# Optimization experiments

Hardware: AMD Instinct MI355X
Metric: run time of the kernel (lower is better)

## Reference

```python
import jax, jax.numpy as jnp
import numpy as np

N, D_IM, D_CLI = 2048, 1024, 64
EPS = 1e-12  # F.normalize eps


def setup_inputs() -> dict:
    key = jax.random.key(0)
    k1, k2, k3, k4 = jax.random.split(key, 4)
    phi_im = jax.random.normal(k1, (N, D_IM), dtype=jnp.float32)
    phi_cli = jax.random.normal(k2, (N, D_CLI), dtype=jnp.float32)
    t = jax.random.randint(k3, (N, 2), 0, 3, dtype=jnp.int64)
    traumatic = jax.random.randint(k4, (N,), 0, 2, dtype=jnp.int64)
    return {"phi_im": phi_im, "phi_cli": phi_cli, "t": t, "traumatic": traumatic}


def _l2norm(x):
    n = jnp.sqrt(jnp.sum(x * x, axis=1, keepdims=True))
    return x / jnp.maximum(n, EPS)


def _pair_block(S, ma, mb):
    # S: [N,N] full cosine similarity; ma, mb: [N] bool group masks.
    valid = ma[:, None] & mb[None, :]
    mat = jnp.where(valid, S, 0.0)            # scatter-into-zero matrix semantics
    masked = jnp.where(valid, S, jnp.inf)     # masked argmin = nearest (least similar) pair
    flat = jnp.argmin(masked.reshape(-1))
    i = flat // S.shape[1]
    j = flat % S.shape[1]
    return mat, masked.reshape(-1)[flat], jnp.stack([i, j])


def reference(phi_im, phi_cli, t, traumatic):
    im_n = _l2norm(phi_im)
    cli_n = _l2norm(phi_cli)
    # single batched GEMM replaces the per-pair python loops
    S_im = im_n @ im_n.T    # [N,N]
    S_cli = cli_n @ cli_n.T  # [N,N]

    t1 = t[:, 1]
    m0 = (t1 == 0) & (traumatic == 1)
    m1 = t1 == 1
    m2 = t1 == 2

    mats, vals, idxs = [], [], []
    for S in (S_im, S_cli):
        for (ma, mb) in ((m0, m1), (m0, m2), (m1, m2)):
            mat, v, ij = _pair_block(S, ma, mb)
            mats.append(mat)
            vals.append(v)
            idxs.append(ij)
    sims = jnp.stack(mats)           # [6, N, N]: im_01, im_02, im_12, cli_01, cli_02, cli_12
    min_vals = jnp.stack(vals)       # [6]
    min_idx = jnp.stack(idxs)        # [6, 2]
    return sims, min_vals, min_idx
```

## Files before the change

### kernel.cpp

```cpp
#include <hip/hip_runtime.h>
#include <stdint.h>

#define NROW 2048
#define D_IM 1024
#define D_CLI 64
#define EPSF 1e-12f
#define NN ((size_t)NROW * (size_t)NROW)

typedef __attribute__((ext_vector_type(8))) short bf16x8;
typedef __attribute__((ext_vector_type(4))) float f32x4;

#define OFF_PACKED   0
#define OFF_CNT      64
#define OFF_CAT      128
#define OFF_LISTS    8320
#define OFF_POS      32896
#define OFF_COLINFO  41216
#define OFF_INVIM    65792
#define OFF_INVCLI   73984
#define OFF_PIM      82176
#define OFF_PCLI     8470784
#define OFF_SC       8995072

__device__ __forceinline__ unsigned int enc_f32(float x) {
    unsigned int u = __float_as_uint(x);
    return (u & 0x80000000u) ? ~u : (u | 0x80000000u);
}
__device__ __forceinline__ unsigned short bf16rn(float x) {
    unsigned int u = __float_as_uint(x);
    return (unsigned short)((u + 0x7FFFu + ((u >> 16) & 1u)) >> 16);
}
__device__ __forceinline__ float bf16tof(unsigned short h) {
    return __uint_as_float(((unsigned int)h) << 16);
}

__global__ __launch_bounds__(256)
void prepscan_kernel(const float* __restrict__ phi_im,
                     const float* __restrict__ phi_cli,
                     const int* __restrict__ t,
                     const int* __restrict__ traumatic,
                     float* __restrict__ inv_im,
                     float* __restrict__ inv_cli,
                     char* __restrict__ pim,
                     char* __restrict__ pcli,
                     int* __restrict__ cnt,
                     int* __restrict__ catArr,
                     int* __restrict__ lists,
                     int* __restrict__ posIn,
                     unsigned int* __restrict__ colinfo,
                     unsigned long long* __restrict__ packed) {
    __shared__ unsigned long long shmem[256];
    const int tid = threadIdx.x;

    if (blockIdx.x == NROW) {
        int cats[8];
        unsigned long long mycnt = 0;
        #pragma unroll
        for (int e = 0; e < 8; e++) {
            int r = tid * 8 + e;
            int t1 = t[2 * r + 1];
            int tr = traumatic[r];
            int c = (t1 == 1) ? 1 : ((t1 == 2) ? 2 : ((tr == 1) ? 0 : 3));
            cats[e] = c;
            catArr[r] = c;
            if (c < 3) mycnt += 1ULL << (21 * c);
        }
        shmem[tid] = mycnt;
        __syncthreads();
        for (int off = 1; off < 256; off <<= 1) {
            unsigned long long v = (tid >= off) ? shmem[tid - off] : 0ULL;
            __syncthreads();
            shmem[tid] += v;
            __syncthreads();
        }
        unsigned long long excl = shmem[tid] - mycnt;
        unsigned long long tot = shmem[255];
        unsigned int loc[3];
        #pragma unroll
        for (int c = 0; c < 3; c++)
            loc[c] = (unsigned int)(excl >> (21 * c)) & 0x1FFFFFu;
        #pragma unroll
        for (int e = 0; e < 8; e++) {
            int r = tid * 8 + e;
            int c = cats[e];
            unsigned int slot = 0xFFFFFFFFu;
            if (c < 3) {
                slot = loc[c]++;
                lists[c * 2048 + slot] = r;
                posIn[r] = (int)slot;
            }
            colinfo[0 * 2048 + r] = (c == 1) ? slot : 0xFFFFFFFFu;
            colinfo[1 * 2048 + r] = (c == 2) ? slot : 0xFFFFFFFFu;
            colinfo[2 * 2048 + r] = (c == 2) ? slot : 0xFFFFFFFFu;
        }
        if (tid == 0) {
            cnt[0] = (int)(tot & 0x1FFFFFu);
            cnt[1] = (int)((tot >> 21) & 0x1FFFFFu);
            cnt[2] = (int)((tot >> 42) & 0x1FFFFFu);
            cnt[3] = 0;
        }
        if (tid < 6) packed[tid] = 0xFFFFFFFFFFFFFFFFULL;
        return;
    }

    float* sred = (float*)shmem;
    const int r = blockIdx.x;

    float4 v = ((const float4*)(phi_im + (size_t)r * D_IM))[tid];
    float a[4] = {v.x, v.y, v.z, v.w};
    unsigned short h4[4], l4[4];
    #pragma unroll
    for (int e = 0; e < 4; e++) {
        h4[e] = bf16rn(a[e]);
        l4[e] = bf16rn(a[e] - bf16tof(h4[e]));
    }
    {
        char* rowb = pim + (size_t)r * 4096 + (tid >> 1) * 32 + (tid & 1) * 8;
        *(ushort4*)rowb = make_ushort4(h4[0], h4[1], h4[2], h4[3]);
        *(ushort4*)(rowb + 16) = make_ushort4(l4[0], l4[1], l4[2], l4[3]);
    }
    sred[tid] = a[0] * a[0] + a[1] * a[1] + a[2] * a[2] + a[3] * a[3];
    __syncthreads();
    for (int off = 128; off > 0; off >>= 1) {
        if (tid < off) sred[tid] += sred[tid + off];
        __syncthreads();
    }
    if (tid == 0) inv_im[r] = 1.0f / fmaxf(sqrtf(sred[0]), EPSF);

    if (tid < 16) {
        float4 c = ((const float4*)(phi_cli + (size_t)r * D_CLI))[tid];
        float b[4] = {c.x, c.y, c.z, c.w};
        unsigned short ch[4], cl[4];
        #pragma unroll
        for (int e = 0; e < 4; e++) {
            ch[e] = bf16rn(b[e]);
            cl[e] = bf16rn(b[e] - bf16tof(ch[e]));
        }
        char* rowb = pcli + (size_t)r * 256 + (tid >> 1) * 32 + (tid & 1) * 8;
        *(ushort4*)rowb = make_ushort4(ch[0], ch[1], ch[2], ch[3]);
        *(ushort4*)(rowb + 16) = make_ushort4(cl[0], cl[1], cl[2], cl[3]);
    }
    if (tid < 64) {
        float c = phi_cli[(size_t)r * D_CLI + tid];
        float cs = c * c;
        #pragma unroll
        for (int off = 32; off > 0; off >>= 1) cs += __shfl_down(cs, off, 64);
        if (tid == 0) inv_cli[r] = 1.0f / fmaxf(sqrtf(cs), EPSF);
    }
}

#define LOAD_SET(s, AH, AL, BH, BL)                                        \
    {                                                                      \
        const int kb_ = (s) * 128;                                         \
        _Pragma("unroll") for (int mt = 0; mt < 4; mt++) {                 \
            AH[mt] = *(const bf16x8*)(pX + offA[mt] + kb_);                \
            AL[mt] = *(const bf16x8*)(pX + offA[mt] + kb_ + 16);           \
            BH[mt] = *(const bf16x8*)(pX + offB[mt] + kb_);                \
            BL[mt] = *(const bf16x8*)(pX + offB[mt] + kb_ + 16);           \
        }                                                                  \
    }
#define MFMA_SET(AH, AL, BH, BL)                                           \
    _Pragma("unroll") for (int mt = 0; mt < 4; mt++)                       \
        _Pragma("unroll") for (int nt = 0; nt < 4; nt++) {                 \
            acc[mt][nt] = __builtin_amdgcn_mfma_f32_16x16x32_bf16(         \
                AH[mt], BH[nt], acc[mt][nt], 0, 0, 0);                     \
            acc[mt][nt] = __builtin_amdgcn_mfma_f32_16x16x32_bf16(         \
                AH[mt], BL[nt], acc[mt][nt], 0, 0, 0);                     \
            acc[mt][nt] = __builtin_amdgcn_mfma_f32_16x16x32_bf16(         \
                AL[mt], BH[nt], acc[mt][nt], 0, 0, 0);                     \
        }

__global__ __launch_bounds__(64, 2)
void gemm_kernel(const char* __restrict__ pim,
                 const char* __restrict__ pcli,
                 const float* __restrict__ inv_im,
                 const float* __restrict__ inv_cli,
                 const int* __restrict__ cnt,
                 const int* __restrict__ lists,
                 unsigned short* __restrict__ Sc,
                 unsigned long long* __restrict__ packed) {
    __shared__ float sIA[64], sIB[64];
    __shared__ int sRA[64], sRB[64];

    const int n0 = cnt[0], n1 = cnt[1], n2 = cnt[2];
    const int tA = (n0 + 63) >> 6, tB = (n1 + 63) >> 6, tC = (n2 + 63) >> 6;
    const int T0 = tA * tB, T1 = tA * tC, T2 = tB * tC;
    const int tot = T0 + T1 + T2;
    int bid = blockIdx.x;
    if (bid >= 2 * tot) return;
    int z = 0;
    if (bid >= tot) { z = 1; bid -= tot; }
    const size_t s0 = (size_t)(tA << 6) * (tB << 6);
    const size_t s1 = (size_t)(tA << 6) * (tC << 6);
    const size_t s2 = (size_t)(tB << 6) * (tC << 6);
    size_t scoff = z ? (s0 + s1 + s2) : 0;
    int gx, nA, nB, nBpad, pp;
    const int *lA, *lB;
    if (bid < T0)           { pp = 0; gx = tB; nA = n0; nB = n1; lA = lists;        lB = lists + 2048; nBpad = tB << 6; }
    else if (bid < T0 + T1) { bid -= T0;      scoff += s0;      pp = 1; gx = tC; nA = n0; nB = n2; lA = lists;        lB = lists + 4096; nBpad = tC << 6; }
    else                    { bid -= T0 + T1; scoff += s0 + s1; pp = 2; gx = tC; nA = n1; nB = n2; lA = lists + 2048; lB = lists + 4096; nBpad = tC << 6; }
    const int by = bid / gx, bx = bid % gx;
    const int i0 = by << 6, j0 = bx << 6;
    const int pz = z * 3 + pp;

    const char* __restrict__ pX = z ? pcli : pim;
    const float* __restrict__ inv = z ? inv_cli : inv_im;
    const int steps = z ? (D_CLI / 32) : (D_IM / 32);
    const size_t stride = z ? 256 : 4096;
    const int lane = threadIdx.x;

    {
        int ia = lA[min(i0 + lane, nA - 1)];
        int ib = lB[min(j0 + lane, nB - 1)];
        sRA[lane] = ia; sRB[lane] = ib;
        sIA[lane] = inv[ia]; sIB[lane] = inv[ib];
    }
    __syncthreads();

    const int mrow = lane & 15;
    const int quad = lane >> 4;
    size_t offA[4], offB[4];
    #pragma unroll
    for (int mt = 0; mt < 4; mt++) {
        offA[mt] = (size_t)sRA[mt * 16 + mrow] * stride + quad * 32;
        offB[mt] = (size_t)sRB[mt * 16 + mrow] * stride + quad * 32;
    }

    f32x4 acc[4][4];
    #pragma unroll
    for (int mt = 0; mt < 4; mt++)
        #pragma unroll
        for (int nt = 0; nt < 4; nt++)
            acc[mt][nt] = (f32x4){0.f, 0.f, 0.f, 0.f};

    bf16x8 A0h[4], A0l[4], B0h[4], B0l[4];
    bf16x8 A1h[4], A1l[4], B1h[4], B1l[4];
    LOAD_SET(0, A0h, A0l, B0h, B0l);
    for (int s = 0; s < steps; s += 2) {
        if (s + 1 < steps) LOAD_SET(s + 1, A1h, A1l, B1h, B1l);
        MFMA_SET(A0h, A0l, B0h, B0l);
        if (s + 2 < steps) LOAD_SET(s + 2, A0h, A0l, B0h, B0l);
        if (s + 1 < steps) MFMA_SET(A1h, A1l, B1h, B1l);
    }

    unsigned long long best = 0xFFFFFFFFFFFFFFFFULL;
    #pragma unroll
    for (int mt = 0; mt < 4; mt++)
        #pragma unroll
        for (int nt = 0; nt < 4; nt++) {
            const int cloc = nt * 16 + mrow;
            const float ivb = sIB[cloc];
            const unsigned int jcol = (unsigned int)sRB[cloc];
            #pragma unroll
            for (int rr = 0; rr < 4; rr++) {
                const int rloc = mt * 16 + quad * 4 + rr;
                float sv = acc[mt][nt][rr] * (sIA[rloc] * ivb);
                Sc[scoff + (size_t)(i0 + rloc) * nBpad + (j0 + cloc)] = bf16rn(sv);
                unsigned long long pk =
                    ((unsigned long long)enc_f32(sv) << 32) |
                    ((unsigned int)sRA[rloc] * (unsigned int)NROW + jcol);
                if (pk < best) best = pk;
            }
        }
    #pragma unroll
    for (int off = 32; off > 0; off >>= 1) {
        unsigned long long o = __shfl_down(best, off, 64);
        if (o < best) best = o;
    }
    if (lane == 0) atomicMin(&packed[pz], best);
}

__global__ __launch_bounds__(256)
void writer_kernel(const unsigned short* __restrict__ Sc,
                   const int* __restrict__ cnt,
                   const int* __restrict__ catArr,
                   const int* __restrict__ posIn,
                   const unsigned int* __restrict__ colinfo,
                   float* __restrict__ out,
                   const unsigned long long* __restrict__ packed) {
    const int b = blockIdx.x;
    const int tid = threadIdx.x;
    if (b == 6 * NROW) {
        const int p = tid;
        if (p < 6) {
            unsigned long long pk = packed[p];
            float v;
            unsigned int flat;
            if (pk == 0xFFFFFFFFFFFFFFFFULL) { v = __builtin_huge_valf(); flat = 0u; }
            else {
                unsigned int key = (unsigned int)(pk >> 32);
                flat = (unsigned int)pk;
                unsigned int bits = (key & 0x80000000u) ? (key ^ 0x80000000u) : ~key;
                v = __uint_as_float(bits);
            }
            out[6 * NN + p] = v;
            out[6 * NN + 6 + 2 * p + 0] = (float)(flat >> 11);
            out[6 * NN + 6 + 2 * p + 1] = (float)(flat & 2047u);
        }
        return;
    }
    const int pz = b >> 11;
    const int row = b & 2047;
    const int z = pz / 3, p = pz - 3 * z;
    float* orow = out + (size_t)pz * NN + (size_t)row * NROW;

    const int rowcat = (p == 2) ? 1 : 0;
    if (catArr[row] != rowcat) {
        const float4 z4 = make_float4(0.f, 0.f, 0.f, 0.f);
        ((float4*)orow)[tid] = z4;
        ((float4*)orow)[tid + 256] = z4;
        return;
    }

    const int n0 = cnt[0], n1 = cnt[1], n2 = cnt[2];
    const int tA = (n0 + 63) >> 6, tB = (n1 + 63) >> 6, tC = (n2 + 63) >> 6;
    const size_t s0 = (size_t)(tA << 6) * (tB << 6);
    const size_t s1 = (size_t)(tA << 6) * (tC << 6);
    const size_t s2 = (size_t)(tB << 6) * (tC << 6);
    size_t scoff = z ? (s0 + s1 + s2) : 0;
    int nBpad;
    if (p == 0)      { nBpad = tB << 6; }
    else if (p == 1) { scoff += s0;      nBpad = tC << 6; }
    else             { scoff += s0 + s1; nBpad = tC << 6; }

    const unsigned short* srow = Sc + scoff + (size_t)posIn[row] * nBpad;
    const uint4* cinfo4 = (const uint4*)(colinfo + p * 2048);

    #pragma unroll
    for (int seg = 0; seg < 2; seg++) {
        const int j4 = tid + seg * 256;
        uint4 inf = cinfo4[j4];
        float v0 = (inf.x != 0xFFFFFFFFu) ? bf16tof(srow[inf.x]) : 0.f;
        float v1 = (inf.y != 0xFFFFFFFFu) ? bf16tof(srow[inf.y]) : 0.f;
        float v2 = (inf.z != 0xFFFFFFFFu) ? bf16tof(srow[inf.z]) : 0.f;
        float v3 = (inf.w != 0xFFFFFFFFu) ? bf16tof(srow[inf.w]) : 0.f;
        ((float4*)orow)[j4] = make_float4(v0, v1, v2, v3);
    }
}

extern "C" void kernel_launch(void* const* d_in, const int* in_sizes, int n_in,
                              void* d_out, int out_size, void* d_ws, size_t ws_size,
                              hipStream_t stream) {
    const float* phi_im = (const float*)d_in[0];
    const float* phi_cli = (const float*)d_in[1];
    const int* t = (const int*)d_in[2];
    const int* traumatic = (const int*)d_in[3];
    float* out = (float*)d_out;

    char* ws = (char*)d_ws;
    unsigned long long* packed = (unsigned long long*)(ws + OFF_PACKED);
    int* cnt = (int*)(ws + OFF_CNT);
    int* catArr = (int*)(ws + OFF_CAT);
    int* lists = (int*)(ws + OFF_LISTS);
    int* posIn = (int*)(ws + OFF_POS);
    unsigned int* colinfo = (unsigned int*)(ws + OFF_COLINFO);
    float* inv_im = (float*)(ws + OFF_INVIM);
    float* inv_cli = (float*)(ws + OFF_INVCLI);
    char* pim = ws + OFF_PIM;
    char* pcli = ws + OFF_PCLI;
    unsigned short* Sc = (unsigned short*)(ws + OFF_SC);

    prepscan_kernel<<<NROW + 1, 256, 0, stream>>>(
        phi_im, phi_cli, t, traumatic, inv_im, inv_cli, pim, pcli,
        cnt, catArr, lists, posIn, colinfo, packed);
    gemm_kernel<<<800, 64, 0, stream>>>(pim, pcli, inv_im, inv_cli,
                                        cnt, lists, Sc, packed);
    writer_kernel<<<6 * NROW + 1, 256, 0, stream>>>(Sc, cnt, catArr, posIn,
                                                    colinfo, out, packed);
}
```

Baseline: 165.6 us.

## Overlap zero-row writes with GEMM and use nontemporal output stores

Zeroing of output rows that fall outside the valid row category moves from the writer kernel into extra blocks appended to the GEMM launch, so those writes can overlap with the GEMM work. The writer kernel now returns early for such rows. Both the zero stores and the gathered value stores use nontemporal builtins to keep the large output stream from polluting cache. The zeroing blocks occupy GPU slots alongside GEMM blocks and could delay GEMM tiles.

```diff
diff --git a/kernel.cpp b/kernel.cpp
--- a/kernel.cpp
+++ b/kernel.cpp
@@ -6,6 +6,7 @@
 #define D_CLI 64
 #define EPSF 1e-12f
 #define NN ((size_t)NROW * (size_t)NROW)
+#define GRID_GEMM 800
 
 typedef __attribute__((ext_vector_type(8))) short bf16x8;
 typedef __attribute__((ext_vector_type(4))) float f32x4;
@@ -177,8 +178,26 @@
                  const float* __restrict__ inv_cli,
                  const int* __restrict__ cnt,
                  const int* __restrict__ lists,
+                 const int* __restrict__ catArr,
                  unsigned short* __restrict__ Sc,
+                 float* __restrict__ out,
                  unsigned long long* __restrict__ packed) {
+    if (blockIdx.x >= GRID_GEMM) {
+        const int b = blockIdx.x - GRID_GEMM;
+        const int pz = b >> 11;
+        const int row = b & 2047;
+        const int p = pz - 3 * (pz / 3);
+        const int rowcat = (p == 2) ? 1 : 0;
+        if (catArr[row] == rowcat) return;
+        float* orow = out + (size_t)pz * NN + (size_t)row * NROW;
+        const int lane = threadIdx.x;
+        const f32x4 z4 = (f32x4){0.f, 0.f, 0.f, 0.f};
+        #pragma unroll
+        for (int s = 0; s < 8; s++)
+            __builtin_nontemporal_store(z4, (f32x4*)orow + lane + s * 64);
+        return;
+    }
+
     __shared__ float sIA[64], sIB[64];
     __shared__ int sRA[64], sRB[64];
 
@@ -302,15 +321,11 @@
     const int pz = b >> 11;
     const int row = b & 2047;
     const int z = pz / 3, p = pz - 3 * z;
+
+    const int rowcat = (p == 2) ? 1 : 0;
+    if (catArr[row] != rowcat) return;
+
     float* orow = out + (size_t)pz * NN + (size_t)row * NROW;
-
-    const int rowcat = (p == 2) ? 1 : 0;
-    if (catArr[row] != rowcat) {
-        const float4 z4 = make_float4(0.f, 0.f, 0.f, 0.f);
-        ((float4*)orow)[tid] = z4;
-        ((float4*)orow)[tid + 256] = z4;
-        return;
-    }
 
     const int n0 = cnt[0], n1 = cnt[1], n2 = cnt[2];
     const int tA = (n0 + 63) >> 6, tB = (n1 + 63) >> 6, tC = (n2 + 63) >> 6;
@@ -330,11 +345,12 @@
     for (int seg = 0; seg < 2; seg++) {
         const int j4 = tid + seg * 256;
         uint4 inf = cinfo4[j4];
-        float v0 = (inf.x != 0xFFFFFFFFu) ? bf16tof(srow[inf.x]) : 0.f;
-        float v1 = (inf.y != 0xFFFFFFFFu) ? bf16tof(srow[inf.y]) : 0.f;
-        float v2 = (inf.z != 0xFFFFFFFFu) ? bf16tof(srow[inf.z]) : 0.f;
-        float v3 = (inf.w != 0xFFFFFFFFu) ? bf16tof(srow[inf.w]) : 0.f;
-        ((float4*)orow)[j4] = make_float4(v0, v1, v2, v3);
+        f32x4 vv;
+        vv[0] = (inf.x != 0xFFFFFFFFu) ? bf16tof(srow[inf.x]) : 0.f;
+        vv[1] = (inf.y != 0xFFFFFFFFu) ? bf16tof(srow[inf.y]) : 0.f;
+        vv[2] = (inf.z != 0xFFFFFFFFu) ? bf16tof(srow[inf.z]) : 0.f;
+        vv[3] = (inf.w != 0xFFFFFFFFu) ? bf16tof(srow[inf.w]) : 0.f;
+        __builtin_nontemporal_store(vv, (f32x4*)orow + j4);
     }
 }
 
@@ -363,8 +379,8 @@
     prepscan_kernel<<<NROW + 1, 256, 0, stream>>>(
         phi_im, phi_cli, t, traumatic, inv_im, inv_cli, pim, pcli,
         cnt, catArr, lists, posIn, colinfo, packed);
-    gemm_kernel<<<800, 64, 0, stream>>>(pim, pcli, inv_im, inv_cli,
-                                        cnt, lists, Sc, packed);
+    gemm_kernel<<<GRID_GEMM + 6 * NROW, 64, 0, stream>>>(
+        pim, pcli, inv_im, inv_cli, cnt, lists, catArr, Sc, out, packed);
     writer_kernel<<<6 * NROW + 1, 256, 0, stream>>>(Sc, cnt, catArr, posIn,
                                                     colinfo, out, packed);
 }
```

Result: no change. 163.4 us (-1.3%).
